# Performance work log

Measured on AMD Instinct MI355X. Metric: run time of the kernel, lower is better.

The kernel has to match this reference:

```python
import jax, jax.numpy as jnp
import numpy as np

B, S, F, H = 256, 1024, 64, 64

def setup_inputs() -> dict:
    key = jax.random.key(0)
    ks = jax.random.split(key, 6)
    x = jax.random.normal(ks[0], (B, S, F), dtype=jnp.float32)
    # Keras LSTM params: kernel [F,4H], recurrent_kernel [H,4H], bias [4H] (gate order i,f,c,o)
    kernel = jax.random.normal(ks[1], (F, 4 * H), dtype=jnp.float32) * (1.0 / np.sqrt(F))
    rec_kernel = jax.random.normal(ks[2], (H, 4 * H), dtype=jnp.float32) * (1.0 / np.sqrt(H))
    bias = jnp.zeros((4 * H,), dtype=jnp.float32)
    dense_w = jax.random.normal(ks[3], (H, 1), dtype=jnp.float32) * (1.0 / np.sqrt(H))
    dense_b = jnp.zeros((1,), dtype=jnp.float32)
    return {"x": x, "kernel": kernel, "rec_kernel": rec_kernel, "bias": bias,
            "dense_w": dense_w, "dense_b": dense_b}

def reference(x, kernel, rec_kernel, bias, dense_w, dense_b):
    # Precompute input contribution for all timesteps: [B,S,4H]
    xz = jnp.einsum('bsf,fg->bsg', x, kernel) + bias
    xz_t = jnp.transpose(xz, (1, 0, 2))  # [S,B,4H]

    def step(carry, xz_step):
        h, c = carry
        z = xz_step + h @ rec_kernel  # [B,4H]
        zi, zf, zc, zo = jnp.split(z, 4, axis=-1)
        i = jax.nn.sigmoid(zi)
        f = jax.nn.sigmoid(zf)
        o = jax.nn.sigmoid(zo)
        c_new = f * c + i * jnp.tanh(zc)
        h_new = o * jnp.tanh(c_new)
        return (h_new, c_new), h_new

    h0 = jnp.zeros((x.shape[0], rec_kernel.shape[0]), dtype=x.dtype)
    c0 = jnp.zeros_like(h0)
    _, hs = jax.lax.scan(step, (h0, c0), xz_t)  # hs: [S,B,H]
    hs = jnp.transpose(hs, (1, 0, 2))  # [B,S,H]
    out = jax.nn.sigmoid(hs @ dense_w + dense_b)  # [B,S,1]
    return out
```

## Files before the change

kernel.cpp:

```cpp
#include <hip/hip_runtime.h>

typedef __attribute__((ext_vector_type(8))) short short8;
typedef __attribute__((ext_vector_type(4))) float f32x4;

#define SS 1024
#define NB 16
#define NBLK 64
#define HROW 72

__device__ __forceinline__ float sigmoidf_(float x) {
    return __builtin_amdgcn_rcpf(1.0f + __expf(-x));
}
__device__ __forceinline__ float tanhf_(float x) {
    return 1.0f - 2.0f * __builtin_amdgcn_rcpf(__expf(2.0f * x) + 1.0f);
}
__device__ __forceinline__ unsigned short f2bf(float f) {
    unsigned int u = __float_as_uint(f);
    u += 0x7fffu + ((u >> 16) & 1u);
    return (unsigned short)(u >> 16);
}

#define RAW_BARRIER() asm volatile("s_waitcnt lgkmcnt(0)\n\ts_barrier" ::: "memory")

__global__ __launch_bounds__(256)
void xconv(const float* __restrict__ x, short* __restrict__ xA) {
    const int gid  = blockIdx.x * 256 + threadIdx.x;
    const int half = gid & 1;
    const int q    = (gid >> 1) & 3;
    const int m    = (gid >> 3) & 15;
    const int bt   = gid >> 7;
    const int t    = bt & 1023;
    const int mb   = bt >> 10;
    const float* __restrict__ xr =
        x + (((size_t)(mb * 16 + m)) * SS + t) * 64 + half * 32 + q * 8;
    const float4 a = *(const float4*)xr;
    const float4 b = *(const float4*)(xr + 4);
    short8 o;
    o[0] = (short)f2bf(a.x); o[1] = (short)f2bf(a.y);
    o[2] = (short)f2bf(a.z); o[3] = (short)f2bf(a.w);
    o[4] = (short)f2bf(b.x); o[5] = (short)f2bf(b.y);
    o[6] = (short)f2bf(b.z); o[7] = (short)f2bf(b.w);
    ((short8*)xA)[gid] = o;
}

#define MF(A, Bv, C) __builtin_amdgcn_mfma_f32_16x16x32_bf16(A, Bv, C, 0, 0, 0)

#define LOADB(VAR, G, KC) do {                                                \
    const float* __restrict__ Wsrc = ((KC) < 2) ? rk : wk;                    \
    const int kb = (((KC) & 1) << 5) + (q << 3);                              \
    const int nn = ((G) << 6) + n0;                                           \
    short8 v;                                                                 \
    v[0] = (short)f2bf(Wsrc[(kb + 0) * 256 + nn]);                            \
    v[1] = (short)f2bf(Wsrc[(kb + 1) * 256 + nn]);                            \
    v[2] = (short)f2bf(Wsrc[(kb + 2) * 256 + nn]);                            \
    v[3] = (short)f2bf(Wsrc[(kb + 3) * 256 + nn]);                            \
    v[4] = (short)f2bf(Wsrc[(kb + 4) * 256 + nn]);                            \
    v[5] = (short)f2bf(Wsrc[(kb + 5) * 256 + nn]);                            \
    v[6] = (short)f2bf(Wsrc[(kb + 6) * 256 + nn]);                            \
    v[7] = (short)f2bf(Wsrc[(kb + 7) * 256 + nn]);                            \
    VAR = v; } while (0)

#define XIDX(T) (xb0 + ((size_t)(T) << 7))

#define REGION(T, PAR, XC0, XC1, XN0, XN1, QC0, QC1, QC2, QC3,                 \
               QN0, QN1, QN2, QN3, DO_O) do {                                  \
    const short8 ha0 = *(const short8*)&hbuf[(PAR) ^ 1][m * HROW + (q << 3)];  \
    const short8 ha1 = *(const short8*)&hbuf[(PAR) ^ 1][m * HROW + 32 + (q << 3)]; \
    { const size_t o = XIDX(((T) + 4 < SS) ? (T) + 4 : SS - 1);                \
      XC0 = xsrc[o]; XC1 = xsrc[o + 1]; }                                      \
    QN0 = MF(XN1, BX01, MF(XN0, BX00, cb0));                                   \
    QN1 = MF(XN1, BX11, MF(XN0, BX10, cb1));                                   \
    QN2 = MF(XN1, BX21, MF(XN0, BX20, cb2));                                   \
    QN3 = MF(XN1, BX31, MF(XN0, BX30, cb3));                                   \
    const f32x4 z0 = MF(ha1, BH01, MF(ha0, BH00, QC0));                        \
    const f32x4 z1 = MF(ha1, BH11, MF(ha0, BH10, QC1));                        \
    const f32x4 z2 = MF(ha1, BH21, MF(ha0, BH20, QC2));                        \
    const f32x4 z3 = MF(ha1, BH31, MF(ha0, BH30, QC3));                        \
    if ((DO_O) && w == 0) {                                                    \
        const f32x4 zzero = {0.f, 0.f, 0.f, 0.f};                              \
        const f32x4 z4 = MF(ha1, BD1, MF(ha0, BD0, zzero));                    \
        if (m == 0) {                                                          \
            out[((size_t)((bb << 2) + q) << 10) + (T) - 1] =                   \
                sigmoidf_(z4[0] + db0);                                        \
        }                                                                      \
    }                                                                          \
    { const float ig = sigmoidf_(z0[0]), fg = sigmoidf_(z1[0]),                \
                  og = sigmoidf_(z3[0]);                                       \
      cc0 = fg * cc0 + ig * tanhf_(z2[0]);                                     \
      const float h0 = og * tanhf_(cc0);                                       \
      hbuf[PAR][(q << 2) * HROW + n0] = (short)f2bf(h0); }                     \
    RAW_BARRIER();                                                             \
} while (0)

__global__ __launch_bounds__(256, 1)
void lstm_pipe(const short* __restrict__ xA, const float* __restrict__ wk,
               const float* __restrict__ rk, const float* __restrict__ bias,
               const float* __restrict__ dw, const float* __restrict__ db,
               float* __restrict__ out) {
    const int bb  = blockIdx.x;
    const int tid = threadIdx.x;
    const int l   = tid & 63;
    const int w   = tid >> 6;
    const int m   = l & 15;
    const int q   = l >> 4;
    const int n0  = (w << 4) + m;

    __shared__ short hbuf[2][16 * HROW];

    for (int i = tid; i < 2 * 16 * HROW; i += 256) ((short*)hbuf)[i] = 0;
    __syncthreads();

    short8 BH00, BH01, BH10, BH11, BH20, BH21, BH30, BH31;
    short8 BX00, BX01, BX10, BX11, BX20, BX21, BX30, BX31;
    LOADB(BH00, 0, 0); LOADB(BH01, 0, 1); LOADB(BX00, 0, 2); LOADB(BX01, 0, 3);
    LOADB(BH10, 1, 0); LOADB(BH11, 1, 1); LOADB(BX10, 1, 2); LOADB(BX11, 1, 3);
    LOADB(BH20, 2, 0); LOADB(BH21, 2, 1); LOADB(BX20, 2, 2); LOADB(BX21, 2, 3);
    LOADB(BH30, 3, 0); LOADB(BH31, 3, 1); LOADB(BX30, 3, 2); LOADB(BX31, 3, 3);

    short8 BD0, BD1;
    {
        short8 v0 = {0, 0, 0, 0, 0, 0, 0, 0}, v1 = v0;
        if (m == 0) {
#pragma unroll
            for (int i = 0; i < 8; ++i) v0[i] = (short)f2bf(dw[(q << 3) + i]);
#pragma unroll
            for (int i = 0; i < 8; ++i) v1[i] = (short)f2bf(dw[32 + (q << 3) + i]);
        }
        BD0 = v0; BD1 = v1;
    }

    const float b0 = bias[n0], b1 = bias[64 + n0];
    const float b2 = bias[128 + n0], b3 = bias[192 + n0];
    const f32x4 cb0 = {b0, b0, b0, b0};
    const f32x4 cb1 = {b1, b1, b1, b1};
    const f32x4 cb2 = {b2, b2, b2, b2};
    const f32x4 cb3 = {b3, b3, b3, b3};
    const float db0 = db[0];

    const int mb  = bb >> 2;
    const int l16 = ((bb & 3) << 2) | (m >> 2);
    const size_t xb0 = (size_t)mb * 131072 + (size_t)(((l16 << 2) | q) << 1);

    const short8* __restrict__ xsrc = (const short8*)xA;
    short8 X00 = xsrc[XIDX(0)], X01 = xsrc[XIDX(0) + 1];
    short8 X10 = xsrc[XIDX(1)], X11 = xsrc[XIDX(1) + 1];
    short8 X20 = xsrc[XIDX(2)], X21 = xsrc[XIDX(2) + 1];
    short8 X30 = xsrc[XIDX(3)], X31 = xsrc[XIDX(3) + 1];

    f32x4 qA0 = MF(X01, BX01, MF(X00, BX00, cb0));
    f32x4 qA1 = MF(X01, BX11, MF(X00, BX10, cb1));
    f32x4 qA2 = MF(X01, BX21, MF(X00, BX20, cb2));
    f32x4 qA3 = MF(X01, BX31, MF(X00, BX30, cb3));
    f32x4 qB0, qB1, qB2, qB3;

    float cc0 = 0.f;

    REGION(0, 0, X00, X01, X10, X11, qA0, qA1, qA2, qA3, qB0, qB1, qB2, qB3, 0);
    REGION(1, 1, X10, X11, X20, X21, qB0, qB1, qB2, qB3, qA0, qA1, qA2, qA3, 1);
    REGION(2, 0, X20, X21, X30, X31, qA0, qA1, qA2, qA3, qB0, qB1, qB2, qB3, 1);
    REGION(3, 1, X30, X31, X00, X01, qB0, qB1, qB2, qB3, qA0, qA1, qA2, qA3, 1);
    for (int t = 4; t < SS; t += 4) {
        REGION(t,     0, X00, X01, X10, X11, qA0, qA1, qA2, qA3, qB0, qB1, qB2, qB3, 1);
        REGION(t + 1, 1, X10, X11, X20, X21, qB0, qB1, qB2, qB3, qA0, qA1, qA2, qA3, 1);
        REGION(t + 2, 0, X20, X21, X30, X31, qA0, qA1, qA2, qA3, qB0, qB1, qB2, qB3, 1);
        REGION(t + 3, 1, X30, X31, X00, X01, qB0, qB1, qB2, qB3, qA0, qA1, qA2, qA3, 1);
    }
    if (w == 0) {
        const short8 ha0 = *(const short8*)&hbuf[1][m * HROW + (q << 3)];
        const short8 ha1 = *(const short8*)&hbuf[1][m * HROW + 32 + (q << 3)];
        const f32x4 zzero = {0.f, 0.f, 0.f, 0.f};
        const f32x4 z4 = MF(ha1, BD1, MF(ha0, BD0, zzero));
        if (m == 0) {
            out[((size_t)((bb << 2) + q) << 10) + SS - 1] =
                sigmoidf_(z4[0] + db0);
        }
    }
}

extern "C" void kernel_launch(void* const* d_in, const int* in_sizes, int n_in,
                              void* d_out, int out_size, void* d_ws, size_t ws_size,
                              hipStream_t stream) {
    const float* x    = (const float*)d_in[0];
    const float* wk   = (const float*)d_in[1];
    const float* rk   = (const float*)d_in[2];
    const float* bias = (const float*)d_in[3];
    const float* dw   = (const float*)d_in[4];
    const float* db   = (const float*)d_in[5];
    float* out = (float*)d_out;

    short* xA = (short*)d_ws;

    hipLaunchKernelGGL(xconv, dim3(NB * 1024 * 128 / 256), dim3(256), 0, stream,
                       x, xA);
    hipLaunchKernelGGL(lstm_pipe, dim3(NBLK), dim3(256), 0, stream,
                       xA, wk, rk, bias, dw, db, out);
}
```

Measured before the change: 437.2 us.

## Precompute input projection in a parallel GEMM kernel, stream fp16 gates to recurrence

Adds an xzgemm kernel that computes x·kernel+bias for all timesteps in parallel with MFMA and stores the result as fp16 in the workspace. The recurrent kernel then reads four precomputed gate pre-activations per step instead of running the input-projection MFMAs on its serial critical path. This halves the per-step MFMA count in the latency-bound loop. In exchange it writes and reads a 128 MB intermediate and adds fp16 rounding of gate pre-activations. The old path is kept as a fallback when the workspace is too small.

```diff
diff --git a/kernel.cpp b/kernel.cpp
--- a/kernel.cpp
+++ b/kernel.cpp
@@ -19,8 +19,181 @@
     u += 0x7fffu + ((u >> 16) & 1u);
     return (unsigned short)(u >> 16);
 }
+__device__ __forceinline__ float h2f_(unsigned short u) {
+    _Float16 h;
+    __builtin_memcpy(&h, &u, 2);
+    return (float)h;
+}
 
 #define RAW_BARRIER() asm volatile("s_waitcnt lgkmcnt(0)\n\ts_barrier" ::: "memory")
+
+#define MF(A, Bv, C) __builtin_amdgcn_mfma_f32_16x16x32_bf16(A, Bv, C, 0, 0, 0)
+
+
+__global__ __launch_bounds__(256)
+void xzgemm(const float* __restrict__ x, const float* __restrict__ wk,
+            const float* __restrict__ bias, _Float16* __restrict__ xz) {
+    const int tid = threadIdx.x;
+    const int l   = tid & 63;
+    const int w   = tid >> 6;
+    const int m   = l & 15;
+    const int q   = l >> 4;
+
+    short8 Bf[16][2];
+    float  bv[16];
+#pragma unroll
+    for (int ct = 0; ct < 16; ++ct) {
+        bv[ct] = bias[ct * 16 + m];
+#pragma unroll
+        for (int h2 = 0; h2 < 2; ++h2) {
+            short8 v;
+#pragma unroll
+            for (int j = 0; j < 8; ++j)
+                v[j] = (short)f2bf(wk[(h2 * 32 + q * 8 + j) * 256 + ct * 16 + m]);
+            Bf[ct][h2] = v;
+        }
+    }
+
+    const int wt = blockIdx.x * 4 + w;
+    for (int it = 0; it < 16; ++it) {
+        const int ti = wt * 16 + it;
+        const float* __restrict__ xr = x + (size_t)(ti * 16 + m) * 64;
+        const float4 a0 = *(const float4*)(xr + q * 8);
+        const float4 a1 = *(const float4*)(xr + q * 8 + 4);
+        const float4 b0 = *(const float4*)(xr + 32 + q * 8);
+        const float4 b1 = *(const float4*)(xr + 32 + q * 8 + 4);
+        short8 xa0, xa1;
+        xa0[0] = (short)f2bf(a0.x); xa0[1] = (short)f2bf(a0.y);
+        xa0[2] = (short)f2bf(a0.z); xa0[3] = (short)f2bf(a0.w);
+        xa0[4] = (short)f2bf(a1.x); xa0[5] = (short)f2bf(a1.y);
+        xa0[6] = (short)f2bf(a1.z); xa0[7] = (short)f2bf(a1.w);
+        xa1[0] = (short)f2bf(b0.x); xa1[1] = (short)f2bf(b0.y);
+        xa1[2] = (short)f2bf(b0.z); xa1[3] = (short)f2bf(b0.w);
+        xa1[4] = (short)f2bf(b1.x); xa1[5] = (short)f2bf(b1.y);
+        xa1[6] = (short)f2bf(b1.z); xa1[7] = (short)f2bf(b1.w);
+
+        _Float16* __restrict__ ob = xz + (size_t)(ti * 16 + q * 4) * 256 + m;
+#pragma unroll
+        for (int ct = 0; ct < 16; ++ct) {
+            const f32x4 c = {bv[ct], bv[ct], bv[ct], bv[ct]};
+            const f32x4 z = MF(xa1, Bf[ct][1], MF(xa0, Bf[ct][0], c));
+            ob[ct * 16 +   0] = (_Float16)z[0];
+            ob[ct * 16 + 256] = (_Float16)z[1];
+            ob[ct * 16 + 512] = (_Float16)z[2];
+            ob[ct * 16 + 768] = (_Float16)z[3];
+        }
+    }
+}
+
+#define LOADB(VAR, G, KC) do {                                                \
+    const int kb = ((KC) << 5) + (q << 3);                                    \
+    const int nn = ((G) << 6) + n0;                                           \
+    short8 v;                                                                 \
+    v[0] = (short)f2bf(rk[(kb + 0) * 256 + nn]);                              \
+    v[1] = (short)f2bf(rk[(kb + 1) * 256 + nn]);                              \
+    v[2] = (short)f2bf(rk[(kb + 2) * 256 + nn]);                              \
+    v[3] = (short)f2bf(rk[(kb + 3) * 256 + nn]);                              \
+    v[4] = (short)f2bf(rk[(kb + 4) * 256 + nn]);                              \
+    v[5] = (short)f2bf(rk[(kb + 5) * 256 + nn]);                              \
+    v[6] = (short)f2bf(rk[(kb + 6) * 256 + nn]);                              \
+    v[7] = (short)f2bf(rk[(kb + 7) * 256 + nn]);                              \
+    VAR = v; } while (0)
+
+#define REGION(T, PAR, P0, P1, P2, P3, DO_O) do {                              \
+    const short8 ha0 = *(const short8*)&hbuf[(PAR) ^ 1][m * HROW + (q << 3)];  \
+    const short8 ha1 = *(const short8*)&hbuf[(PAR) ^ 1][m * HROW + 32 + (q << 3)]; \
+    const float f0 = h2f_(P0), f1 = h2f_(P1), f2 = h2f_(P2), f3 = h2f_(P3);    \
+    const f32x4 ci = {f0, f0, f0, f0};                                         \
+    const f32x4 cf = {f1, f1, f1, f1};                                         \
+    const f32x4 cg = {f2, f2, f2, f2};                                         \
+    const f32x4 co = {f3, f3, f3, f3};                                         \
+    const f32x4 z0 = MF(ha1, BH01, MF(ha0, BH00, ci));                         \
+    const f32x4 z1 = MF(ha1, BH11, MF(ha0, BH10, cf));                         \
+    const f32x4 z2 = MF(ha1, BH21, MF(ha0, BH20, cg));                         \
+    const f32x4 z3 = MF(ha1, BH31, MF(ha0, BH30, co));                         \
+    { const size_t xo = (size_t)(((T) + 2 < SS) ? (T) + 2 : SS - 1) << 8;      \
+      P0 = xzl[xo];       P1 = xzl[xo + 64];                                   \
+      P2 = xzl[xo + 128]; P3 = xzl[xo + 192]; }                                \
+    if ((DO_O) && w == 0) {                                                    \
+        const f32x4 zzero = {0.f, 0.f, 0.f, 0.f};                              \
+        const f32x4 z4 = MF(ha1, BD1, MF(ha0, BD0, zzero));                    \
+        if (m == 0) {                                                          \
+            out[((size_t)((bb << 2) + q) << 10) + (T) - 1] =                   \
+                sigmoidf_(z4[0] + db0);                                        \
+        }                                                                      \
+    }                                                                          \
+    { const float ig = sigmoidf_(z0[0]), fg = sigmoidf_(z1[0]),                \
+                  og = sigmoidf_(z3[0]);                                       \
+      cc0 = fg * cc0 + ig * tanhf_(z2[0]);                                     \
+      const float h0 = og * tanhf_(cc0);                                       \
+      hbuf[PAR][(q << 2) * HROW + n0] = (short)f2bf(h0); }                     \
+    RAW_BARRIER();                                                             \
+} while (0)
+
+__global__ __launch_bounds__(256, 1)
+void lstm_xz(const unsigned short* __restrict__ xz, const float* __restrict__ rk,
+             const float* __restrict__ dw, const float* __restrict__ db,
+             float* __restrict__ out) {
+    const int bb  = blockIdx.x;
+    const int tid = threadIdx.x;
+    const int l   = tid & 63;
+    const int w   = tid >> 6;
+    const int m   = l & 15;
+    const int q   = l >> 4;
+    const int n0  = (w << 4) + m;
+
+    __shared__ short hbuf[2][16 * HROW];
+
+    for (int i = tid; i < 2 * 16 * HROW; i += 256) ((short*)hbuf)[i] = 0;
+    __syncthreads();
+
+    short8 BH00, BH01, BH10, BH11, BH20, BH21, BH30, BH31;
+    LOADB(BH00, 0, 0); LOADB(BH01, 0, 1);
+    LOADB(BH10, 1, 0); LOADB(BH11, 1, 1);
+    LOADB(BH20, 2, 0); LOADB(BH21, 2, 1);
+    LOADB(BH30, 3, 0); LOADB(BH31, 3, 1);
+
+    short8 BD0, BD1;
+    {
+        short8 v0 = {0, 0, 0, 0, 0, 0, 0, 0}, v1 = v0;
+        if (m == 0) {
+#pragma unroll
+            for (int i = 0; i < 8; ++i) v0[i] = (short)f2bf(dw[(q << 3) + i]);
+#pragma unroll
+            for (int i = 0; i < 8; ++i) v1[i] = (short)f2bf(dw[32 + (q << 3) + i]);
+        }
+        BD0 = v0; BD1 = v1;
+    }
+    const float db0 = db[0];
+
+    const unsigned short* __restrict__ xzl =
+        xz + ((size_t)((bb << 2) + q) << 18) + n0;
+
+    unsigned short pA0 = xzl[0],   pA1 = xzl[64];
+    unsigned short pA2 = xzl[128], pA3 = xzl[192];
+    unsigned short pB0 = xzl[256 +   0], pB1 = xzl[256 +  64];
+    unsigned short pB2 = xzl[256 + 128], pB3 = xzl[256 + 192];
+
+    float cc0 = 0.f;
+
+    REGION(0, 0, pA0, pA1, pA2, pA3, 0);
+    REGION(1, 1, pB0, pB1, pB2, pB3, 1);
+    for (int t = 2; t < SS; t += 2) {
+        REGION(t,     0, pA0, pA1, pA2, pA3, 1);
+        REGION(t + 1, 1, pB0, pB1, pB2, pB3, 1);
+    }
+    if (w == 0) {
+        const short8 ha0 = *(const short8*)&hbuf[1][m * HROW + (q << 3)];
+        const short8 ha1 = *(const short8*)&hbuf[1][m * HROW + 32 + (q << 3)];
+        const f32x4 zzero = {0.f, 0.f, 0.f, 0.f};
+        const f32x4 z4 = MF(ha1, BD1, MF(ha0, BD0, zzero));
+        if (m == 0) {
+            out[((size_t)((bb << 2) + q) << 10) + SS - 1] =
+                sigmoidf_(z4[0] + db0);
+        }
+    }
+}
+
 
 __global__ __launch_bounds__(256)
 void xconv(const float* __restrict__ x, short* __restrict__ xA) {
@@ -43,9 +216,7 @@
     ((short8*)xA)[gid] = o;
 }
 
-#define MF(A, Bv, C) __builtin_amdgcn_mfma_f32_16x16x32_bf16(A, Bv, C, 0, 0, 0)
-
-#define LOADB(VAR, G, KC) do {                                                \
+#define LOADB_FB(VAR, G, KC) do {                                             \
     const float* __restrict__ Wsrc = ((KC) < 2) ? rk : wk;                    \
     const int kb = (((KC) & 1) << 5) + (q << 3);                              \
     const int nn = ((G) << 6) + n0;                                           \
@@ -62,7 +233,7 @@
 
 #define XIDX(T) (xb0 + ((size_t)(T) << 7))
 
-#define REGION(T, PAR, XC0, XC1, XN0, XN1, QC0, QC1, QC2, QC3,                 \
+#define REGION_FB(T, PAR, XC0, XC1, XN0, XN1, QC0, QC1, QC2, QC3,              \
                QN0, QN1, QN2, QN3, DO_O) do {                                  \
     const short8 ha0 = *(const short8*)&hbuf[(PAR) ^ 1][m * HROW + (q << 3)];  \
     const short8 ha1 = *(const short8*)&hbuf[(PAR) ^ 1][m * HROW + 32 + (q << 3)]; \
@@ -93,10 +264,10 @@
 } while (0)
 
 __global__ __launch_bounds__(256, 1)
-void lstm_pipe(const short* __restrict__ xA, const float* __restrict__ wk,
-               const float* __restrict__ rk, const float* __restrict__ bias,
-               const float* __restrict__ dw, const float* __restrict__ db,
-               float* __restrict__ out) {
+void lstm_fb(const short* __restrict__ xA, const float* __restrict__ wk,
+             const float* __restrict__ rk, const float* __restrict__ bias,
+             const float* __restrict__ dw, const float* __restrict__ db,
+             float* __restrict__ out) {
     const int bb  = blockIdx.x;
     const int tid = threadIdx.x;
     const int l   = tid & 63;
@@ -112,10 +283,10 @@
 
     short8 BH00, BH01, BH10, BH11, BH20, BH21, BH30, BH31;
     short8 BX00, BX01, BX10, BX11, BX20, BX21, BX30, BX31;
-    LOADB(BH00, 0, 0); LOADB(BH01, 0, 1); LOADB(BX00, 0, 2); LOADB(BX01, 0, 3);
-    LOADB(BH10, 1, 0); LOADB(BH11, 1, 1); LOADB(BX10, 1, 2); LOADB(BX11, 1, 3);
-    LOADB(BH20, 2, 0); LOADB(BH21, 2, 1); LOADB(BX20, 2, 2); LOADB(BX21, 2, 3);
-    LOADB(BH30, 3, 0); LOADB(BH31, 3, 1); LOADB(BX30, 3, 2); LOADB(BX31, 3, 3);
+    LOADB_FB(BH00, 0, 0); LOADB_FB(BH01, 0, 1); LOADB_FB(BX00, 0, 2); LOADB_FB(BX01, 0, 3);
+    LOADB_FB(BH10, 1, 0); LOADB_FB(BH11, 1, 1); LOADB_FB(BX10, 1, 2); LOADB_FB(BX11, 1, 3);
+    LOADB_FB(BH20, 2, 0); LOADB_FB(BH21, 2, 1); LOADB_FB(BX20, 2, 2); LOADB_FB(BX21, 2, 3);
+    LOADB_FB(BH30, 3, 0); LOADB_FB(BH31, 3, 1); LOADB_FB(BX30, 3, 2); LOADB_FB(BX31, 3, 3);
 
     short8 BD0, BD1;
     {
@@ -155,15 +326,15 @@
 
     float cc0 = 0.f;
 
-    REGION(0, 0, X00, X01, X10, X11, qA0, qA1, qA2, qA3, qB0, qB1, qB2, qB3, 0);
-    REGION(1, 1, X10, X11, X20, X21, qB0, qB1, qB2, qB3, qA0, qA1, qA2, qA3, 1);
-    REGION(2, 0, X20, X21, X30, X31, qA0, qA1, qA2, qA3, qB0, qB1, qB2, qB3, 1);
-    REGION(3, 1, X30, X31, X00, X01, qB0, qB1, qB2, qB3, qA0, qA1, qA2, qA3, 1);
+    REGION_FB(0, 0, X00, X01, X10, X11, qA0, qA1, qA2, qA3, qB0, qB1, qB2, qB3, 0);
+    REGION_FB(1, 1, X10, X11, X20, X21, qB0, qB1, qB2, qB3, qA0, qA1, qA2, qA3, 1);
+    REGION_FB(2, 0, X20, X21, X30, X31, qA0, qA1, qA2, qA3, qB0, qB1, qB2, qB3, 1);
+    REGION_FB(3, 1, X30, X31, X00, X01, qB0, qB1, qB2, qB3, qA0, qA1, qA2, qA3, 1);
     for (int t = 4; t < SS; t += 4) {
-        REGION(t,     0, X00, X01, X10, X11, qA0, qA1, qA2, qA3, qB0, qB1, qB2, qB3, 1);
-        REGION(t + 1, 1, X10, X11, X20, X21, qB0, qB1, qB2, qB3, qA0, qA1, qA2, qA3, 1);
-        REGION(t + 2, 0, X20, X21, X30, X31, qA0, qA1, qA2, qA3, qB0, qB1, qB2, qB3, 1);
-        REGION(t + 3, 1, X30, X31, X00, X01, qB0, qB1, qB2, qB3, qA0, qA1, qA2, qA3, 1);
+        REGION_FB(t,     0, X00, X01, X10, X11, qA0, qA1, qA2, qA3, qB0, qB1, qB2, qB3, 1);
+        REGION_FB(t + 1, 1, X10, X11, X20, X21, qB0, qB1, qB2, qB3, qA0, qA1, qA2, qA3, 1);
+        REGION_FB(t + 2, 0, X20, X21, X30, X31, qA0, qA1, qA2, qA3, qB0, qB1, qB2, qB3, 1);
+        REGION_FB(t + 3, 1, X30, X31, X00, X01, qB0, qB1, qB2, qB3, qA0, qA1, qA2, qA3, 1);
     }
     if (w == 0) {
         const short8 ha0 = *(const short8*)&hbuf[1][m * HROW + (q << 3)];
@@ -188,10 +359,19 @@
     const float* db   = (const float*)d_in[5];
     float* out = (float*)d_out;
 
-    short* xA = (short*)d_ws;
-
-    hipLaunchKernelGGL(xconv, dim3(NB * 1024 * 128 / 256), dim3(256), 0, stream,
-                       x, xA);
-    hipLaunchKernelGGL(lstm_pipe, dim3(NBLK), dim3(256), 0, stream,
-                       xA, wk, rk, bias, dw, db, out);
-}
+    const size_t XZ_BYTES = (size_t)256 * 1024 * 256 * sizeof(_Float16);
+
+    if (ws_size >= XZ_BYTES) {
+        _Float16* xz = (_Float16*)d_ws;
+        hipLaunchKernelGGL(xzgemm, dim3(256), dim3(256), 0, stream,
+                           x, wk, bias, xz);
+        hipLaunchKernelGGL(lstm_xz, dim3(NBLK), dim3(256), 0, stream,
+                           (const unsigned short*)xz, rk, dw, db, out);
+    } else {
+        short* xA = (short*)d_ws;
+        hipLaunchKernelGGL(xconv, dim3(NB * 1024 * 128 / 256), dim3(256), 0,
+                           stream, x, xA);
+        hipLaunchKernelGGL(lstm_fb, dim3(NBLK), dim3(256), 0, stream,
+                           xA, wk, rk, bias, dw, db, out);
+    }
+}
```

Result: slower. 513.4 us (+17.4%).

## Precompute input projection in a separate GEMM kernel and slim the recurrent loop

Applied to the files above, without the earlier changes.

Moves the x·W_kernel + bias projection out of the sequential LSTM loop into a parallel MFMA GEMM kernel that writes packed fp16 gate pre-activations to workspace. The recurrent kernel then loads one uint2 per step instead of running 8 extra MFMAs. When the workspace is large enough, the per-step dense output head is also moved to a separate kernel fed by stored h values. This shortens the serial critical path per timestep, at the cost of a large fp16 intermediate (about 128 MB) and extra global traffic, plus some added fp16 rounding of the projected inputs.

```diff
diff --git a/kernel.cpp b/kernel.cpp
--- a/kernel.cpp
+++ b/kernel.cpp
@@ -4,7 +4,6 @@
 typedef __attribute__((ext_vector_type(4))) float f32x4;
 
 #define SS 1024
-#define NB 16
 #define NBLK 64
 #define HROW 72
 
@@ -19,84 +18,145 @@
     u += 0x7fffu + ((u >> 16) & 1u);
     return (unsigned short)(u >> 16);
 }
+__device__ __forceinline__ float bf2f(unsigned short u) {
+    return __uint_as_float((unsigned int)u << 16);
+}
+__device__ __forceinline__ float h2f_lo(unsigned int u) {
+    _Float16 h; unsigned short s = (unsigned short)(u & 0xffffu);
+    __builtin_memcpy(&h, &s, 2); return (float)h;
+}
+__device__ __forceinline__ float h2f_hi(unsigned int u) {
+    _Float16 h; unsigned short s = (unsigned short)(u >> 16);
+    __builtin_memcpy(&h, &s, 2); return (float)h;
+}
+__device__ __forceinline__ unsigned int pkf16(float a, float b) {
+    auto p = __builtin_amdgcn_cvt_pkrtz(a, b);
+    unsigned int u; __builtin_memcpy(&u, &p, 4); return u;
+}
 
 #define RAW_BARRIER() asm volatile("s_waitcnt lgkmcnt(0)\n\ts_barrier" ::: "memory")
 
+#define MF(A, Bv, C) __builtin_amdgcn_mfma_f32_16x16x32_bf16(A, Bv, C, 0, 0, 0)
+
 __global__ __launch_bounds__(256)
-void xconv(const float* __restrict__ x, short* __restrict__ xA) {
-    const int gid  = blockIdx.x * 256 + threadIdx.x;
-    const int half = gid & 1;
-    const int q    = (gid >> 1) & 3;
-    const int m    = (gid >> 3) & 15;
-    const int bt   = gid >> 7;
-    const int t    = bt & 1023;
-    const int mb   = bt >> 10;
-    const float* __restrict__ xr =
-        x + (((size_t)(mb * 16 + m)) * SS + t) * 64 + half * 32 + q * 8;
-    const float4 a = *(const float4*)xr;
-    const float4 b = *(const float4*)(xr + 4);
-    short8 o;
-    o[0] = (short)f2bf(a.x); o[1] = (short)f2bf(a.y);
-    o[2] = (short)f2bf(a.z); o[3] = (short)f2bf(a.w);
-    o[4] = (short)f2bf(b.x); o[5] = (short)f2bf(b.y);
-    o[6] = (short)f2bf(b.z); o[7] = (short)f2bf(b.w);
-    ((short8*)xA)[gid] = o;
-}
-
-#define MF(A, Bv, C) __builtin_amdgcn_mfma_f32_16x16x32_bf16(A, Bv, C, 0, 0, 0)
+void xzgemm(const float* __restrict__ x, const float* __restrict__ wk,
+            const float* __restrict__ bias, uint2* __restrict__ xzp) {
+    const int tid = threadIdx.x;
+    const int l   = tid & 63;
+    const int w   = tid >> 6;
+    const int m   = l & 15;
+    const int q   = l >> 4;
+
+    short8 Bf[16][2];
+    float  bv[16];
+#pragma unroll
+    for (int ct = 0; ct < 16; ++ct) {
+        bv[ct] = bias[ct * 16 + m];
+#pragma unroll
+        for (int h2 = 0; h2 < 2; ++h2) {
+            short8 v;
+#pragma unroll
+            for (int j = 0; j < 8; ++j)
+                v[j] = (short)f2bf(wk[(h2 * 32 + q * 8 + j) * 256 + ct * 16 + m]);
+            Bf[ct][h2] = v;
+        }
+    }
+
+    const int wt = blockIdx.x * 4 + w;
+    for (int it = 0; it < 16; ++it) {
+        const int ti = wt * 16 + it;
+        const float* __restrict__ xr = x + (size_t)(ti * 16 + m) * 64;
+        const float4 a0 = *(const float4*)(xr + q * 8);
+        const float4 a1 = *(const float4*)(xr + q * 8 + 4);
+        const float4 b0 = *(const float4*)(xr + 32 + q * 8);
+        const float4 b1 = *(const float4*)(xr + 32 + q * 8 + 4);
+        short8 xa0, xa1;
+        xa0[0] = (short)f2bf(a0.x); xa0[1] = (short)f2bf(a0.y);
+        xa0[2] = (short)f2bf(a0.z); xa0[3] = (short)f2bf(a0.w);
+        xa0[4] = (short)f2bf(a1.x); xa0[5] = (short)f2bf(a1.y);
+        xa0[6] = (short)f2bf(a1.z); xa0[7] = (short)f2bf(a1.w);
+        xa1[0] = (short)f2bf(b0.x); xa1[1] = (short)f2bf(b0.y);
+        xa1[2] = (short)f2bf(b0.z); xa1[3] = (short)f2bf(b0.w);
+        xa1[4] = (short)f2bf(b1.x); xa1[5] = (short)f2bf(b1.y);
+        xa1[6] = (short)f2bf(b1.z); xa1[7] = (short)f2bf(b1.w);
+
+#pragma unroll
+        for (int ctn = 0; ctn < 4; ++ctn) {
+            const f32x4 ci = {bv[ctn],      bv[ctn],      bv[ctn],      bv[ctn]};
+            const f32x4 cf = {bv[ctn + 4],  bv[ctn + 4],  bv[ctn + 4],  bv[ctn + 4]};
+            const f32x4 cc = {bv[ctn + 8],  bv[ctn + 8],  bv[ctn + 8],  bv[ctn + 8]};
+            const f32x4 co = {bv[ctn + 12], bv[ctn + 12], bv[ctn + 12], bv[ctn + 12]};
+            const f32x4 zi = MF(xa1, Bf[ctn][1],      MF(xa0, Bf[ctn][0],      ci));
+            const f32x4 zf = MF(xa1, Bf[ctn + 4][1],  MF(xa0, Bf[ctn + 4][0],  cf));
+            const f32x4 zc = MF(xa1, Bf[ctn + 8][1],  MF(xa0, Bf[ctn + 8][0],  cc));
+            const f32x4 zo = MF(xa1, Bf[ctn + 12][1], MF(xa0, Bf[ctn + 12][0], co));
+            uint2* __restrict__ ob =
+                xzp + ((size_t)(ti * 16 + q * 4) * 64 + ctn * 16 + m);
+#pragma unroll
+            for (int r = 0; r < 4; ++r) {
+                uint2 v;
+                v.x = pkf16(zi[r], zf[r]);
+                v.y = pkf16(zc[r], zo[r]);
+                ob[(size_t)r * 64] = v;
+            }
+        }
+    }
+}
 
 #define LOADB(VAR, G, KC) do {                                                \
-    const float* __restrict__ Wsrc = ((KC) < 2) ? rk : wk;                    \
-    const int kb = (((KC) & 1) << 5) + (q << 3);                              \
+    const int kb = ((KC) << 5) + (q << 3);                                    \
     const int nn = ((G) << 6) + n0;                                           \
     short8 v;                                                                 \
-    v[0] = (short)f2bf(Wsrc[(kb + 0) * 256 + nn]);                            \
-    v[1] = (short)f2bf(Wsrc[(kb + 1) * 256 + nn]);                            \
-    v[2] = (short)f2bf(Wsrc[(kb + 2) * 256 + nn]);                            \
-    v[3] = (short)f2bf(Wsrc[(kb + 3) * 256 + nn]);                            \
-    v[4] = (short)f2bf(Wsrc[(kb + 4) * 256 + nn]);                            \
-    v[5] = (short)f2bf(Wsrc[(kb + 5) * 256 + nn]);                            \
-    v[6] = (short)f2bf(Wsrc[(kb + 6) * 256 + nn]);                            \
-    v[7] = (short)f2bf(Wsrc[(kb + 7) * 256 + nn]);                            \
+    v[0] = (short)f2bf(rk[(kb + 0) * 256 + nn]);                              \
+    v[1] = (short)f2bf(rk[(kb + 1) * 256 + nn]);                              \
+    v[2] = (short)f2bf(rk[(kb + 2) * 256 + nn]);                              \
+    v[3] = (short)f2bf(rk[(kb + 3) * 256 + nn]);                              \
+    v[4] = (short)f2bf(rk[(kb + 4) * 256 + nn]);                              \
+    v[5] = (short)f2bf(rk[(kb + 5) * 256 + nn]);                              \
+    v[6] = (short)f2bf(rk[(kb + 6) * 256 + nn]);                              \
+    v[7] = (short)f2bf(rk[(kb + 7) * 256 + nn]);                              \
     VAR = v; } while (0)
 
-#define XIDX(T) (xb0 + ((size_t)(T) << 7))
-
-#define REGION(T, PAR, XC0, XC1, XN0, XN1, QC0, QC1, QC2, QC3,                 \
-               QN0, QN1, QN2, QN3, DO_O) do {                                  \
+#define REGION(T, PAR, P, DO_O) do {                                           \
     const short8 ha0 = *(const short8*)&hbuf[(PAR) ^ 1][m * HROW + (q << 3)];  \
     const short8 ha1 = *(const short8*)&hbuf[(PAR) ^ 1][m * HROW + 32 + (q << 3)]; \
-    { const size_t o = XIDX(((T) + 4 < SS) ? (T) + 4 : SS - 1);                \
-      XC0 = xsrc[o]; XC1 = xsrc[o + 1]; }                                      \
-    QN0 = MF(XN1, BX01, MF(XN0, BX00, cb0));                                   \
-    QN1 = MF(XN1, BX11, MF(XN0, BX10, cb1));                                   \
-    QN2 = MF(XN1, BX21, MF(XN0, BX20, cb2));                                   \
-    QN3 = MF(XN1, BX31, MF(XN0, BX30, cb3));                                   \
-    const f32x4 z0 = MF(ha1, BH01, MF(ha0, BH00, QC0));                        \
-    const f32x4 z1 = MF(ha1, BH11, MF(ha0, BH10, QC1));                        \
-    const f32x4 z2 = MF(ha1, BH21, MF(ha0, BH20, QC2));                        \
-    const f32x4 z3 = MF(ha1, BH31, MF(ha0, BH30, QC3));                        \
-    if ((DO_O) && w == 0) {                                                    \
-        const f32x4 zzero = {0.f, 0.f, 0.f, 0.f};                              \
-        const f32x4 z4 = MF(ha1, BD1, MF(ha0, BD0, zzero));                    \
+    const uint2 cur = P;                                                       \
+    P = xb[(size_t)(((T) + 2 < SS) ? (T) + 2 : SS - 1) << 6];                  \
+    const float vi = h2f_lo(cur.x), vf = h2f_hi(cur.x);                        \
+    const float vc = h2f_lo(cur.y), vo = h2f_hi(cur.y);                        \
+    const f32x4 cgi = {vi, vi, vi, vi};                                        \
+    const f32x4 cgf = {vf, vf, vf, vf};                                        \
+    const f32x4 cgc = {vc, vc, vc, vc};                                        \
+    const f32x4 cgo = {vo, vo, vo, vo};                                        \
+    const f32x4 zc = MF(ha1, BHC1, MF(ha0, BHC0, cgc));                        \
+    const f32x4 zo = MF(ha1, BHO1, MF(ha0, BHO0, cgo));                        \
+    const f32x4 zi = MF(ha1, BHI1, MF(ha0, BHI0, cgi));                        \
+    const f32x4 zf = MF(ha1, BHF1, MF(ha0, BHF0, cgf));                        \
+    if (DM == 1 && (DO_O) && w == 0) {                                         \
+        const f32x4 zz = {0.f, 0.f, 0.f, 0.f};                                 \
+        const f32x4 z4 = MF(ha1, BD1, MF(ha0, BD0, zz));                       \
         if (m == 0) {                                                          \
             out[((size_t)((bb << 2) + q) << 10) + (T) - 1] =                   \
                 sigmoidf_(z4[0] + db0);                                        \
         }                                                                      \
     }                                                                          \
-    { const float ig = sigmoidf_(z0[0]), fg = sigmoidf_(z1[0]),                \
-                  og = sigmoidf_(z3[0]);                                       \
-      cc0 = fg * cc0 + ig * tanhf_(z2[0]);                                     \
-      const float h0 = og * tanhf_(cc0);                                       \
-      hbuf[PAR][(q << 2) * HROW + n0] = (short)f2bf(h0); }                     \
+    const float tc = tanhf_(zc[0]);                                            \
+    const float go = sigmoidf_(zo[0]);                                         \
+    const float gi = sigmoidf_(zi[0]);                                         \
+    const float gf = sigmoidf_(zf[0]);                                         \
+    cc0 = gf * cc0 + gi * tc;                                                  \
+    const float h0 = go * tanhf_(cc0);                                         \
+    const unsigned short hb16 = f2bf(h0);                                      \
+    hbuf[PAR][(q << 2) * HROW + n0] = (short)hb16;                             \
+    if (DM == 0) hb[(size_t)(T) << 6] = hb16;                                  \
     RAW_BARRIER();                                                             \
 } while (0)
 
+template<int DM>
 __global__ __launch_bounds__(256, 1)
-void lstm_pipe(const short* __restrict__ xA, const float* __restrict__ wk,
-               const float* __restrict__ rk, const float* __restrict__ bias,
-               const float* __restrict__ dw, const float* __restrict__ db,
-               float* __restrict__ out) {
+void lstm_xz(const uint2* __restrict__ xzu, const float* __restrict__ rk,
+             unsigned short* __restrict__ hg, const float* __restrict__ dw,
+             const float* __restrict__ db, float* __restrict__ out) {
     const int bb  = blockIdx.x;
     const int tid = threadIdx.x;
     const int l   = tid & 63;
@@ -110,12 +170,11 @@
     for (int i = tid; i < 2 * 16 * HROW; i += 256) ((short*)hbuf)[i] = 0;
     __syncthreads();
 
-    short8 BH00, BH01, BH10, BH11, BH20, BH21, BH30, BH31;
-    short8 BX00, BX01, BX10, BX11, BX20, BX21, BX30, BX31;
-    LOADB(BH00, 0, 0); LOADB(BH01, 0, 1); LOADB(BX00, 0, 2); LOADB(BX01, 0, 3);
-    LOADB(BH10, 1, 0); LOADB(BH11, 1, 1); LOADB(BX10, 1, 2); LOADB(BX11, 1, 3);
-    LOADB(BH20, 2, 0); LOADB(BH21, 2, 1); LOADB(BX20, 2, 2); LOADB(BX21, 2, 3);
-    LOADB(BH30, 3, 0); LOADB(BH31, 3, 1); LOADB(BX30, 3, 2); LOADB(BX31, 3, 3);
+    short8 BHI0, BHI1, BHF0, BHF1, BHC0, BHC1, BHO0, BHO1;
+    LOADB(BHI0, 0, 0); LOADB(BHI1, 0, 1);
+    LOADB(BHF0, 1, 0); LOADB(BHF1, 1, 1);
+    LOADB(BHC0, 2, 0); LOADB(BHC1, 2, 1);
+    LOADB(BHO0, 3, 0); LOADB(BHO1, 3, 1);
 
     short8 BD0, BD1;
     {
@@ -128,53 +187,48 @@
         }
         BD0 = v0; BD1 = v1;
     }
-
-    const float b0 = bias[n0], b1 = bias[64 + n0];
-    const float b2 = bias[128 + n0], b3 = bias[192 + n0];
-    const f32x4 cb0 = {b0, b0, b0, b0};
-    const f32x4 cb1 = {b1, b1, b1, b1};
-    const f32x4 cb2 = {b2, b2, b2, b2};
-    const f32x4 cb3 = {b3, b3, b3, b3};
     const float db0 = db[0];
 
-    const int mb  = bb >> 2;
-    const int l16 = ((bb & 3) << 2) | (m >> 2);
-    const size_t xb0 = (size_t)mb * 131072 + (size_t)(((l16 << 2) | q) << 1);
-
-    const short8* __restrict__ xsrc = (const short8*)xA;
-    short8 X00 = xsrc[XIDX(0)], X01 = xsrc[XIDX(0) + 1];
-    short8 X10 = xsrc[XIDX(1)], X11 = xsrc[XIDX(1) + 1];
-    short8 X20 = xsrc[XIDX(2)], X21 = xsrc[XIDX(2) + 1];
-    short8 X30 = xsrc[XIDX(3)], X31 = xsrc[XIDX(3) + 1];
-
-    f32x4 qA0 = MF(X01, BX01, MF(X00, BX00, cb0));
-    f32x4 qA1 = MF(X01, BX11, MF(X00, BX10, cb1));
-    f32x4 qA2 = MF(X01, BX21, MF(X00, BX20, cb2));
-    f32x4 qA3 = MF(X01, BX31, MF(X00, BX30, cb3));
-    f32x4 qB0, qB1, qB2, qB3;
-
+    const size_t base = ((size_t)((bb << 2) + q) << 16) + n0;
+    const uint2* __restrict__ xb = xzu + base;
+    unsigned short* __restrict__ hb = hg + base;
+
+    uint2 PA = xb[0], PB = xb[64];
     float cc0 = 0.f;
 
-    REGION(0, 0, X00, X01, X10, X11, qA0, qA1, qA2, qA3, qB0, qB1, qB2, qB3, 0);
-    REGION(1, 1, X10, X11, X20, X21, qB0, qB1, qB2, qB3, qA0, qA1, qA2, qA3, 1);
-    REGION(2, 0, X20, X21, X30, X31, qA0, qA1, qA2, qA3, qB0, qB1, qB2, qB3, 1);
-    REGION(3, 1, X30, X31, X00, X01, qB0, qB1, qB2, qB3, qA0, qA1, qA2, qA3, 1);
-    for (int t = 4; t < SS; t += 4) {
-        REGION(t,     0, X00, X01, X10, X11, qA0, qA1, qA2, qA3, qB0, qB1, qB2, qB3, 1);
-        REGION(t + 1, 1, X10, X11, X20, X21, qB0, qB1, qB2, qB3, qA0, qA1, qA2, qA3, 1);
-        REGION(t + 2, 0, X20, X21, X30, X31, qA0, qA1, qA2, qA3, qB0, qB1, qB2, qB3, 1);
-        REGION(t + 3, 1, X30, X31, X00, X01, qB0, qB1, qB2, qB3, qA0, qA1, qA2, qA3, 1);
-    }
-    if (w == 0) {
+    REGION(0, 0, PA, 0);
+    REGION(1, 1, PB, 1);
+    for (int t = 2; t < SS; t += 2) {
+        REGION(t,     0, PA, 1);
+        REGION(t + 1, 1, PB, 1);
+    }
+    if (DM == 1 && w == 0) {
         const short8 ha0 = *(const short8*)&hbuf[1][m * HROW + (q << 3)];
         const short8 ha1 = *(const short8*)&hbuf[1][m * HROW + 32 + (q << 3)];
-        const f32x4 zzero = {0.f, 0.f, 0.f, 0.f};
-        const f32x4 z4 = MF(ha1, BD1, MF(ha0, BD0, zzero));
+        const f32x4 zz = {0.f, 0.f, 0.f, 0.f};
+        const f32x4 z4 = MF(ha1, BD1, MF(ha0, BD0, zz));
         if (m == 0) {
             out[((size_t)((bb << 2) + q) << 10) + SS - 1] =
                 sigmoidf_(z4[0] + db0);
         }
     }
+}
+
+__global__ __launch_bounds__(256)
+void dense_out(const unsigned short* __restrict__ hg,
+               const float* __restrict__ dw, const float* __restrict__ db,
+               float* __restrict__ out) {
+    const int row = blockIdx.x * 256 + threadIdx.x;
+    const short8* __restrict__ hr = (const short8*)(hg + (size_t)row * 64);
+    float acc = db[0];
+#pragma unroll
+    for (int jj = 0; jj < 8; ++jj) {
+        const short8 v = hr[jj];
+#pragma unroll
+        for (int k = 0; k < 8; ++k)
+            acc += bf2f((unsigned short)v[k]) * dw[jj * 8 + k];
+    }
+    out[row] = sigmoidf_(acc);
 }
 
 extern "C" void kernel_launch(void* const* d_in, const int* in_sizes, int n_in,
@@ -188,10 +242,21 @@
     const float* db   = (const float*)d_in[5];
     float* out = (float*)d_out;
 
-    short* xA = (short*)d_ws;
-
-    hipLaunchKernelGGL(xconv, dim3(NB * 1024 * 128 / 256), dim3(256), 0, stream,
-                       x, xA);
-    hipLaunchKernelGGL(lstm_pipe, dim3(NBLK), dim3(256), 0, stream,
-                       xA, wk, rk, bias, dw, db, out);
-}
+    const size_t XZ_BYTES = (size_t)262144 * 256 * 2;
+    const size_t HG_BYTES = (size_t)262144 * 64 * 2;
+
+    uint2* xz = (uint2*)d_ws;
+    hipLaunchKernelGGL(xzgemm, dim3(256), dim3(256), 0, stream,
+                       x, wk, bias, xz);
+
+    if (ws_size >= XZ_BYTES + HG_BYTES) {
+        unsigned short* hg = (unsigned short*)((char*)d_ws + XZ_BYTES);
+        hipLaunchKernelGGL((lstm_xz<0>), dim3(NBLK), dim3(256), 0, stream,
+                           xz, rk, hg, dw, db, out);
+        hipLaunchKernelGGL(dense_out, dim3(1024), dim3(256), 0, stream,
+                           hg, dw, db, out);
+    } else {
+        hipLaunchKernelGGL((lstm_xz<1>), dim3(NBLK), dim3(256), 0, stream,
+                           xz, rk, (unsigned short*)nullptr, dw, db, out);
+    }
+}
```

Measured after the change: 426.7 us. -2.4%, faster.
